# Performance work log

Hardware: AMD Instinct MI355X
Metric: run time of the kernel (lower is better)

The kernel has to match this reference:

```python
import jax, jax.numpy as jnp
import numpy as np

C0 = 256
GROUP = C0 // 32  # 8 groups, 32 channels each
K = 9             # 3x3 kernel
PAD = 1

def _layernorm(x, g, b):
    m = jnp.mean(x, -1, keepdims=True)
    v = jnp.var(x, -1, keepdims=True)
    return (x - m) * jax.lax.rsqrt(v + 1e-5) * g + b

def _dwconv(x, w, b):
    # depthwise 3x3, NHWC, kernel [3,3,1,C]
    y = jax.lax.conv_general_dilated(x, w, (1, 1), 'SAME', dimension_numbers=('NHWC', 'HWIO', 'NHWC'), feature_group_count=x.shape[-1])
    return y + b

def _bilinear(img, ix, iy):
    # img [B,Hp,Wp,c]; ix,iy [B,L] pixel coords; bilinear, zeros padding, align_corners=False
    B, Hp, Wp, c = img.shape
    flat = img.reshape(B, Hp * Wp, c)
    x0 = jnp.floor(ix)
    y0 = jnp.floor(iy)
    tx = ix - x0
    ty = iy - y0
    out = jnp.zeros(ix.shape + (c,), img.dtype)
    for dx, dy, w in ((0, 0, (1 - tx) * (1 - ty)), (1, 0, tx * (1 - ty)), (0, 1, (1 - tx) * ty), (1, 1, tx * ty)):
        xi = x0 + dx
        yi = y0 + dy
        valid = (xi >= 0) & (xi < Wp) & (yi >= 0) & (yi < Hp)
        idx = (jnp.clip(yi, 0, Hp - 1) * Wp + jnp.clip(xi, 0, Wp - 1)).astype(jnp.int32)
        v = jax.vmap(lambda f, i: f[i])(flat, idx)  # [B,L,c]
        out = out + v * (w * valid)[..., None]
    return out

def _dcnv3(x, dw_w, dw_b, ln_g, ln_b, in_w, in_b, off_w, off_b, mk_w, mk_b, out_w, out_b):
    # x: [N,H,W,C] channel-last, DCNv3 core (stride=1, dilation=1, offset_scale=1)
    N, H, W, C = x.shape
    G = GROUP
    gc = C // G
    v = x @ in_w + in_b  # input_proj (value)
    # offset/mask branch: dwconv -> LN -> GELU
    f = jax.nn.gelu(_layernorm(_dwconv(x, dw_w, dw_b), ln_g, ln_b), approximate=False)
    offset = (f @ off_w + off_b).reshape(N, H, W, G, K, 2)
    mask = jax.nn.softmax((f @ mk_w + mk_b).reshape(N, H, W, G, K), axis=-1)
    Hp = H + 2 * PAD
    Wp = W + 2 * PAD
    vp = jnp.pad(v, ((0, 0), (PAD, PAD), (PAD, PAD), (0, 0)))
    # reference points normalized by padded spatial size
    ref_x = (jnp.arange(W, dtype=x.dtype) + PAD + 0.5) / Wp
    ref_y = (jnp.arange(H, dtype=x.dtype) + PAD + 0.5) / Hp
    rx, ry = jnp.meshgrid(ref_x, ref_y, indexing='xy')  # [H,W]
    ref = jnp.stack([rx, ry], -1)  # [H,W,2] (x,y)
    k = jnp.arange(3, dtype=x.dtype) - 1.0  # [-1,0,1]
    gx, gy = jnp.meshgrid(k / Wp, k / Hp, indexing='ij')
    kgrid = jnp.stack([gx, gy], -1).reshape(K, 2)
    norm = jnp.array([Wp, Hp], dtype=x.dtype)
    loc = ref[None, :, :, None, None, :] + kgrid[None, None, None, None, :, :] + offset / norm  # [N,H,W,G,K,2]
    sg = (2.0 * loc - 1.0).transpose(0, 3, 1, 2, 4, 5).reshape(N * G, H * W * K, 2)
    ix = ((sg[..., 0] + 1.0) * Wp - 1.0) * 0.5
    iy = ((sg[..., 1] + 1.0) * Hp - 1.0) * 0.5
    imgs = vp.reshape(N, Hp, Wp, G, gc).transpose(0, 3, 1, 2, 4).reshape(N * G, Hp, Wp, gc)
    samp = _bilinear(imgs, ix, iy).reshape(N, G, H * W, K, gc)
    m = mask.transpose(0, 3, 1, 2, 4).reshape(N, G, H * W, K)
    out = jnp.einsum('nglkc,nglk->nglc', samp, m)
    out = out.transpose(0, 2, 1, 3).reshape(N, H, W, C)
    return out @ out_w + out_b

def setup_inputs() -> dict:
    key = jax.random.key(0)
    ks = iter(jax.random.split(key, 40))
    C, G = C0, GROUP
    d = {"x": jax.random.normal(next(ks), (2, C, 64, 64), jnp.float32)}
    for p in ("a", "b"):
        d[p + "_dw_w"] = jax.random.normal(next(ks), (3, 3, 1, C), jnp.float32) * 0.05
        d[p + "_dw_b"] = jnp.zeros((C,), jnp.float32)
        d[p + "_ln_g"] = jnp.ones((C,), jnp.float32)
        d[p + "_ln_b"] = jnp.zeros((C,), jnp.float32)
        d[p + "_in_w"] = jax.random.normal(next(ks), (C, C), jnp.float32) * 0.0625
        d[p + "_in_b"] = jnp.zeros((C,), jnp.float32)
        d[p + "_off_w"] = jax.random.normal(next(ks), (C, G * K * 2), jnp.float32) * 0.02
        d[p + "_off_b"] = jnp.zeros((G * K * 2,), jnp.float32)
        d[p + "_mk_w"] = jax.random.normal(next(ks), (C, G * K), jnp.float32) * 0.02
        d[p + "_mk_b"] = jnp.zeros((G * K,), jnp.float32)
        d[p + "_out_w"] = jax.random.normal(next(ks), (C, C), jnp.float32) * 0.0625
        d[p + "_out_b"] = jnp.zeros((C,), jnp.float32)
    d["proj_w"] = jax.random.normal(next(ks), (C, C), jnp.float32) * 0.0625
    d["proj_b"] = jnp.zeros((C,), jnp.float32)
    return d

def reference(x, a_dw_w, a_dw_b, a_ln_g, a_ln_b, a_in_w, a_in_b, a_off_w, a_off_b, a_mk_w, a_mk_b, a_out_w, a_out_b, b_dw_w, b_dw_b, b_ln_g, b_ln_b, b_in_w, b_in_b, b_off_w, b_off_b, b_mk_w, b_mk_b, b_out_w, b_out_b, proj_w, proj_b):
    x1 = x.transpose(0, 2, 3, 1)  # NCHW -> NHWC
    attn1 = _dcnv3(x1, a_dw_w, a_dw_b, a_ln_g, a_ln_b, a_in_w, a_in_b, a_off_w, a_off_b, a_mk_w, a_mk_b, a_out_w, a_out_b)
    attn2 = _dcnv3(attn1, b_dw_w, b_dw_b, b_ln_g, b_ln_b, b_in_w, b_in_b, b_off_w, b_off_b, b_mk_w, b_mk_b, b_out_w, b_out_b)
    attn = attn2 @ proj_w + proj_b
    return x * attn.transpose(0, 3, 1, 2)
```

## Files before the change

kernel.cpp:

```cpp
#include <hip/hip_runtime.h>
#include <hip/hip_bf16.h>
#include <math.h>

#define HH 64
#define WW 64
#define CH 256
#define NB 2
#define HWSZ (HH*WW)
#define PIX (NB*HWSZ)

typedef __attribute__((ext_vector_type(8))) short bf16x8;
typedef __attribute__((ext_vector_type(4))) float f32x4;

static __device__ __forceinline__ ushort f2bf(float f){
  union { __hip_bfloat16 h; ushort u; } cv;
  cv.h = __float2bfloat16(f);
  return cv.u;
}
static __device__ __forceinline__ float bflo(uint u){ return __uint_as_float(u << 16); }
static __device__ __forceinline__ float bfhi(uint u){ return __uint_as_float(u & 0xffff0000u); }

__global__ __launch_bounds__(256) void k_prep(const float* __restrict__ x,
    ushort* __restrict__ out16,
    const float* __restrict__ a_in_w, const float* __restrict__ a_off_w,
    const float* __restrict__ a_mk_w, const float* __restrict__ a_out_w,
    const float* __restrict__ b_in_w, const float* __restrict__ b_off_w,
    const float* __restrict__ b_mk_w, const float* __restrict__ b_out_w,
    const float* __restrict__ proj_w, ushort* __restrict__ Bt,
    const float* __restrict__ a_off_b, const float* __restrict__ a_mk_b,
    const float* __restrict__ b_off_b, const float* __restrict__ b_mk_b,
    float* __restrict__ bcatA, float* __restrict__ bcatB){
  __shared__ float t[32][33];
  int b = blockIdx.x;
  int tid = threadIdx.x;
  int tx = tid & 31, ty = tid >> 5;
  if (b < 2048) {
    int n = b >> 10, rem = b & 1023;
    int p0 = (rem & 127) * 32, c0 = (rem >> 7) * 32;
    const float* inn = x + (size_t)n * CH * HWSZ;
    ushort* o16 = out16 + (size_t)n * HWSZ * CH;
    #pragma unroll
    for (int i = 0; i < 4; ++i) {
      int c = c0 + ty + i*8;
      t[ty + i*8][tx] = inn[(size_t)c * HWSZ + p0 + tx];
    }
    __syncthreads();
    #pragma unroll
    for (int i = 0; i < 4; ++i) {
      int p = p0 + ty + i*8;
      o16[(size_t)p * CH + c0 + tx] = f2bf(t[tx][ty + i*8]);
    }
  } else if (b < 2496) {
    int zz = b - 2048;
    int z = zz >> 6, rem = zz & 63;
    int n0 = (rem & 7) * 32, k0 = (rem >> 3) * 32;
    const float* W = a_in_w; int mode = 0;
    switch(z){
      case 0: W = a_in_w; break;
      case 1: mode = 1; break;
      case 2: W = a_out_w; break;
      case 3: W = b_in_w; break;
      case 4: mode = 2; break;
      case 5: W = b_out_w; break;
      default: W = proj_w; break;
    }
    #pragma unroll
    for (int i = 0; i < 4; ++i) {
      int k = k0 + ty + i*8, nn = n0 + tx;
      float val;
      if (mode == 0) val = W[k*256 + nn];
      else {
        const float* ow = (mode == 1) ? a_off_w : b_off_w;
        const float* mw = (mode == 1) ? a_mk_w  : b_mk_w;
        val = (nn < 144) ? ow[k*144 + nn] : ((nn < 216) ? mw[k*72 + nn - 144] : 0.f);
      }
      t[ty + i*8][tx] = val;
    }
    __syncthreads();
    #pragma unroll
    for (int i = 0; i < 4; ++i) {
      int nn = n0 + ty + i*8, k = k0 + tx;
      Bt[(size_t)z*65536 + nn*256 + k] = f2bf(t[tx][ty + i*8]);
    }
  } else {
    bcatA[tid] = (tid < 144) ? a_off_b[tid] : ((tid < 216) ? a_mk_b[tid-144] : 0.f);
    bcatB[tid] = (tid < 144) ? b_off_b[tid] : ((tid < 216) ? b_mk_b[tid-144] : 0.f);
  }
}

__global__ __launch_bounds__(256) void k_dwln(const ushort* __restrict__ xin,
    const float* __restrict__ dw_w, const float* __restrict__ dw_b,
    const float* __restrict__ ln_g, const float* __restrict__ ln_b,
    ushort* __restrict__ f){
  int w_ = threadIdx.x >> 6, l = threadIdx.x & 63;
  int pix = blockIdx.x * 4 + w_;
  int c = l << 2;
  int n  = pix >> 12;
  int hw = pix & 4095;
  int h = hw >> 6, w = hw & 63;
  const ushort* xb = xin + (size_t)n * HWSZ * CH;
  float4 bv = *reinterpret_cast<const float4*>(&dw_b[c]);
  float s0 = bv.x, s1 = bv.y, s2 = bv.z, s3 = bv.w;
  #pragma unroll
  for (int i = 0; i < 3; ++i) {
    int y = h + i - 1;
    if ((unsigned)y < 64u) {
      #pragma unroll
      for (int j = 0; j < 3; ++j) {
        int x = w + j - 1;
        if ((unsigned)x < 64u) {
          uint2 xv = *reinterpret_cast<const uint2*>(&xb[((size_t)((y<<6)+x))*CH + c]);
          float4 wv = *reinterpret_cast<const float4*>(&dw_w[(i*3+j)*CH + c]);
          s0 = fmaf(bflo(xv.x), wv.x, s0);
          s1 = fmaf(bfhi(xv.x), wv.y, s1);
          s2 = fmaf(bflo(xv.y), wv.z, s2);
          s3 = fmaf(bfhi(xv.y), wv.w, s3);
        }
      }
    }
  }
  float v1 = s0 + s1 + s2 + s3;
  float v2 = s0*s0 + s1*s1 + s2*s2 + s3*s3;
  #pragma unroll
  for (int off = 32; off >= 1; off >>= 1) {
    v1 += __shfl_xor(v1, off);
    v2 += __shfl_xor(v2, off);
  }
  float mean = v1 * (1.f/256.f);
  float var  = v2 * (1.f/256.f) - mean*mean;
  float inv  = rsqrtf(var + 1e-5f);
  float4 gv = *reinterpret_cast<const float4*>(&ln_g[c]);
  float4 bb = *reinterpret_cast<const float4*>(&ln_b[c]);
  float z0 = (s0 - mean) * inv * gv.x + bb.x;
  float z1 = (s1 - mean) * inv * gv.y + bb.y;
  float z2 = (s2 - mean) * inv * gv.z + bb.z;
  float z3 = (s3 - mean) * inv * gv.w + bb.w;
  float g0 = 0.5f * z0 * (1.f + erff(z0 * 0.70710678118654752f));
  float g1 = 0.5f * z1 * (1.f + erff(z1 * 0.70710678118654752f));
  float g2 = 0.5f * z2 * (1.f + erff(z2 * 0.70710678118654752f));
  float g3 = 0.5f * z3 * (1.f + erff(z3 * 0.70710678118654752f));
  uint2 pk;
  pk.x = (uint)f2bf(g0) | ((uint)f2bf(g1) << 16);
  pk.y = (uint)f2bf(g2) | ((uint)f2bf(g3) << 16);
  *reinterpret_cast<uint2*>(&f[(size_t)pix*CH + c]) = pk;
}

template<int MODE>
static __device__ __forceinline__ void gemm_core(ushort* As, ushort* Bs,
    int rows, int by, const ushort* __restrict__ Bt, const float* __restrict__ bias,
    float* __restrict__ Cf, ushort* __restrict__ Cb,
    const float* __restrict__ xg, float* __restrict__ outg){
  int tid = threadIdx.x;
  int w = tid >> 6, l = tid & 63;
  int lr = l & 15, lk = l >> 4;
  int br = tid >> 2, bc2 = (tid & 3) << 1;
  const ushort* Bg = Bt + (size_t)(by*64 + br) * 256 + ((tid & 3) << 4);
  uint4 pb0 = *reinterpret_cast<const uint4*>(Bg);
  uint4 pb1 = *reinterpret_cast<const uint4*>(Bg + 8);
  f32x4 acc[4] = {};
  #pragma unroll
  for (int ph = 0; ph < 4; ++ph) {
    __syncthreads();
    *reinterpret_cast<uint4*>(&Bs[(br << 6) + (((bc2    ) ^ (br & 7)) << 3)]) = pb0;
    *reinterpret_cast<uint4*>(&Bs[(br << 6) + (((bc2 + 1) ^ (br & 7)) << 3)]) = pb1;
    __syncthreads();
    if (ph < 3) {
      pb0 = *reinterpret_cast<const uint4*>(Bg + (ph+1)*64);
      pb1 = *reinterpret_cast<const uint4*>(Bg + (ph+1)*64 + 8);
    }
    #pragma unroll
    for (int ks = 0; ks < 2; ++ks) {
      int col = w*16 + lr;
      bf16x8 bf = *reinterpret_cast<const bf16x8*>(&Bs[(col << 6) + ((((ks<<2) + lk) ^ (col & 7)) << 3)]);
      #pragma unroll
      for (int mi = 0; mi < 4; ++mi) {
        int row = mi*16 + lr;
        int ck = ((ph<<3) + (ks<<2) + lk) ^ (row & 31);
        bf16x8 af = *reinterpret_cast<const bf16x8*>(&As[(row << 8) + (ck << 3)]);
        acc[mi] = __builtin_amdgcn_mfma_f32_16x16x32_bf16(af, bf, acc[mi], 0, 0, 0);
      }
    }
  }
  int colg = by*64 + w*16 + lr;
  float bval = bias[colg];
  #pragma unroll
  for (int mi = 0; mi < 4; ++mi) {
    int row0 = rows + mi*16 + (lk << 2);
    if (MODE == 3) {
      int n = row0 >> 12, hw = row0 & 4095;
      size_t base = (size_t)n * (CH*HWSZ) + (size_t)colg * HWSZ + hw;
      float4 xv = *reinterpret_cast<const float4*>(&xg[base]);
      float4 ov;
      ov.x = xv.x * (acc[mi][0] + bval);
      ov.y = xv.y * (acc[mi][1] + bval);
      ov.z = xv.z * (acc[mi][2] + bval);
      ov.w = xv.w * (acc[mi][3] + bval);
      *reinterpret_cast<float4*>(&outg[base]) = ov;
    } else {
      #pragma unroll
      for (int j = 0; j < 4; ++j) {
        float val = acc[mi][j] + bval;
        if (MODE == 2) Cf[(size_t)(row0 + j) * 256 + colg] = val;
        else           Cb[(size_t)(row0 + j) * 256 + colg] = f2bf(val);
      }
    }
  }
}

static __device__ __forceinline__ void stage_A(ushort* As, const ushort* __restrict__ A, int rows){
  int tid = threadIdx.x;
  int r = tid >> 2, q0 = (tid & 3) << 3;
  const ushort* Ag = A + (size_t)(rows + r) * 256 + (q0 << 3);
  #pragma unroll
  for (int i = 0; i < 8; ++i) {
    uint4 v = *reinterpret_cast<const uint4*>(Ag + (i << 3));
    *reinterpret_cast<uint4*>(&As[(r << 8) + (((q0 + i) ^ (r & 31)) << 3)]) = v;
  }
}

template<int MODE>
__global__ __launch_bounds__(256, 4) void k_gemm256(const ushort* __restrict__ A,
    const ushort* __restrict__ Bt, const float* __restrict__ bias,
    float* __restrict__ Cf, ushort* __restrict__ Cb,
    const float* __restrict__ xg, float* __restrict__ outg){
  __shared__ ushort As[64*256];
  __shared__ ushort Bs[64*64];
  int rows = blockIdx.x * 64, by = blockIdx.y;
  stage_A(As, A, rows);
  gemm_core<MODE>(As, Bs, rows, by, Bt, bias, Cf, Cb, xg, outg);
}

__global__ __launch_bounds__(256, 4) void k_vfm(
    const ushort* __restrict__ Av, const ushort* __restrict__ Btv,
    const float* __restrict__ biasv, ushort* __restrict__ v16,
    const ushort* __restrict__ Af, const ushort* __restrict__ Btf,
    const float* __restrict__ biasf, float* __restrict__ fm32){
  __shared__ ushort As[64*256];
  __shared__ ushort Bs[64*64];
  int rows = blockIdx.x * 64, by = blockIdx.y;
  if (blockIdx.z == 0) {
    stage_A(As, Av, rows);
    gemm_core<0>(As, Bs, rows, by, Btv, biasv, nullptr, v16, nullptr, nullptr);
  } else {
    stage_A(As, Af, rows);
    gemm_core<2>(As, Bs, rows, by, Btf, biasf, fm32, nullptr, nullptr, nullptr);
  }
}

__global__ __launch_bounds__(256, 4) void k_sample(const ushort* __restrict__ v,
    const float* __restrict__ fm, ushort* __restrict__ o){
  __shared__ float sfm[4][256];
  int wv = threadIdx.x >> 6, l = threadIdx.x & 63;
  int pix = blockIdx.x * 4 + wv;
  int c = l << 2;
  int g = l >> 3;
  *reinterpret_cast<float4*>(&sfm[wv][c]) = *reinterpret_cast<const float4*>(&fm[(size_t)pix*256 + c]);
  __syncthreads();
  const float* fp = sfm[wv];
  float ml[9];
  float mx = -1e30f;
  #pragma unroll
  for (int k = 0; k < 9; ++k) { ml[k] = fp[144 + g*9 + k]; mx = fmaxf(mx, ml[k]); }
  float ssum = 0.f;
  #pragma unroll
  for (int k = 0; k < 9; ++k) { ml[k] = __expf(ml[k] - mx); ssum += ml[k]; }
  int n = pix >> 12;
  int hw = pix & 4095;
  int h = hw >> 6, w = hw & 63;
  const ushort* vb = v + (size_t)n * HWSZ * CH + c;
  float a0 = 0.f, a1 = 0.f, a2 = 0.f, a3 = 0.f;
  #pragma unroll
  for (int k = 0; k < 9; ++k) {
    int dx = k/3 - 1, dy = k%3 - 1;
    float ox = fp[g*18 + k*2];
    float oy = fp[g*18 + k*2 + 1];
    float xu = (float)(w + dx) + ox;
    float yu = (float)(h + dy) + oy;
    float xf = floorf(xu), yf = floorf(yu);
    float tx = xu - xf, ty = yu - yf;
    int x0 = (int)xf, y0 = (int)yf;
    int x1 = x0 + 1, y1 = y0 + 1;
    float m00 = (float)((unsigned)x0 < 64u && (unsigned)y0 < 64u);
    float m10 = (float)((unsigned)x1 < 64u && (unsigned)y0 < 64u);
    float m01 = (float)((unsigned)x0 < 64u && (unsigned)y1 < 64u);
    float m11 = (float)((unsigned)x1 < 64u && (unsigned)y1 < 64u);
    int xc0 = min(max(x0, 0), 63), xc1 = min(max(x1, 0), 63);
    int yc0 = min(max(y0, 0), 63), yc1 = min(max(y1, 0), 63);
    float w0x = 1.f - tx, w0y = 1.f - ty;
    uint2 q00 = *reinterpret_cast<const uint2*>(vb + (((yc0 << 6) + xc0) << 8));
    uint2 q10 = *reinterpret_cast<const uint2*>(vb + (((yc0 << 6) + xc1) << 8));
    uint2 q01 = *reinterpret_cast<const uint2*>(vb + (((yc1 << 6) + xc0) << 8));
    uint2 q11 = *reinterpret_cast<const uint2*>(vb + (((yc1 << 6) + xc1) << 8));
    float w00 = ml[k] * (w0x * w0y * m00);
    float w10 = ml[k] * (tx  * w0y * m10);
    float w01 = ml[k] * (w0x * ty  * m01);
    float w11 = ml[k] * (tx  * ty  * m11);
    a0 = fmaf(bflo(q00.x), w00, a0); a1 = fmaf(bfhi(q00.x), w00, a1);
    a2 = fmaf(bflo(q00.y), w00, a2); a3 = fmaf(bfhi(q00.y), w00, a3);
    a0 = fmaf(bflo(q10.x), w10, a0); a1 = fmaf(bfhi(q10.x), w10, a1);
    a2 = fmaf(bflo(q10.y), w10, a2); a3 = fmaf(bfhi(q10.y), w10, a3);
    a0 = fmaf(bflo(q01.x), w01, a0); a1 = fmaf(bfhi(q01.x), w01, a1);
    a2 = fmaf(bflo(q01.y), w01, a2); a3 = fmaf(bfhi(q01.y), w01, a3);
    a0 = fmaf(bflo(q11.x), w11, a0); a1 = fmaf(bfhi(q11.x), w11, a1);
    a2 = fmaf(bflo(q11.y), w11, a2); a3 = fmaf(bfhi(q11.y), w11, a3);
  }
  float inv = 1.f / ssum;
  uint2 pk;
  pk.x = (uint)f2bf(a0 * inv) | ((uint)f2bf(a1 * inv) << 16);
  pk.y = (uint)f2bf(a2 * inv) | ((uint)f2bf(a3 * inv) << 16);
  *reinterpret_cast<uint2*>(&o[(size_t)pix*256 + c]) = pk;
}

extern "C" void kernel_launch(void* const* d_in, const int* in_sizes, int n_in,
                              void* d_out, int out_size, void* d_ws, size_t ws_size,
                              hipStream_t stream) {
  const float* x      = (const float*)d_in[0];
  const float* a_dw_w = (const float*)d_in[1];
  const float* a_dw_b = (const float*)d_in[2];
  const float* a_ln_g = (const float*)d_in[3];
  const float* a_ln_b = (const float*)d_in[4];
  const float* a_in_w = (const float*)d_in[5];
  const float* a_in_b = (const float*)d_in[6];
  const float* a_off_w= (const float*)d_in[7];
  const float* a_off_b= (const float*)d_in[8];
  const float* a_mk_w = (const float*)d_in[9];
  const float* a_mk_b = (const float*)d_in[10];
  const float* a_out_w= (const float*)d_in[11];
  const float* a_out_b= (const float*)d_in[12];
  const float* b_dw_w = (const float*)d_in[13];
  const float* b_dw_b = (const float*)d_in[14];
  const float* b_ln_g = (const float*)d_in[15];
  const float* b_ln_b = (const float*)d_in[16];
  const float* b_in_w = (const float*)d_in[17];
  const float* b_in_b = (const float*)d_in[18];
  const float* b_off_w= (const float*)d_in[19];
  const float* b_off_b= (const float*)d_in[20];
  const float* b_mk_w = (const float*)d_in[21];
  const float* b_mk_b = (const float*)d_in[22];
  const float* b_out_w= (const float*)d_in[23];
  const float* b_out_b= (const float*)d_in[24];
  const float* proj_w = (const float*)d_in[25];
  const float* proj_b = (const float*)d_in[26];
  float* out = (float*)d_out;

  const size_t BUF = (size_t)PIX * CH;
  float* fm32   = (float*)d_ws;
  ushort* u = (ushort*)(fm32 + BUF);
  ushort* bx16 = u;  u += BUF;
  ushort* f16  = u;  u += BUF;
  ushort* v16  = u;  u += BUF;
  ushort* o16  = u;  u += BUF;
  ushort* a116 = u;  u += BUF;
  ushort* a216 = u;  u += BUF;
  ushort* Btw  = u;  u += (size_t)7*65536;
  float* bcatA = (float*)u;
  float* bcatB = bcatA + 256;

  dim3 gvfm(PIX/64, 4, 2);
  dim3 ggem(PIX/64, 4);

  k_prep<<<2497, 256, 0, stream>>>(x, bx16,
      a_in_w, a_off_w, a_mk_w, a_out_w, b_in_w, b_off_w, b_mk_w, b_out_w, proj_w, Btw,
      a_off_b, a_mk_b, b_off_b, b_mk_b, bcatA, bcatB);

  k_dwln<<<PIX/4, 256, 0, stream>>>(bx16, a_dw_w, a_dw_b, a_ln_g, a_ln_b, f16);
  k_vfm<<<gvfm, 256, 0, stream>>>(bx16, Btw + 0*65536, a_in_b, v16,
                                  f16, Btw + 1*65536, bcatA, fm32);
  k_sample<<<PIX/4, 256, 0, stream>>>(v16, fm32, o16);
  k_gemm256<0><<<ggem, 256, 0, stream>>>(o16, Btw + 2*65536, a_out_b, nullptr, a116, nullptr, nullptr);

  k_dwln<<<PIX/4, 256, 0, stream>>>(a116, b_dw_w, b_dw_b, b_ln_g, b_ln_b, f16);
  k_vfm<<<gvfm, 256, 0, stream>>>(a116, Btw + 3*65536, b_in_b, v16,
                                  f16, Btw + 4*65536, bcatB, fm32);
  k_sample<<<PIX/4, 256, 0, stream>>>(v16, fm32, o16);
  k_gemm256<0><<<ggem, 256, 0, stream>>>(o16, Btw + 5*65536, b_out_b, nullptr, a216, nullptr, nullptr);

  k_gemm256<3><<<ggem, 256, 0, stream>>>(a216, Btw + 6*65536, proj_b, nullptr, nullptr, x, out);
}
```

Baseline: 95.41 us.

## Fuse depthwise conv + LayerNorm + GELU into the offset/mask GEMM blocks

Removes the separate k_dwln kernel and its bf16 intermediate buffer. A fifth y-slice of the k_vfm grid now computes the dwconv/LN/GELU for its 64 pixels directly into the swizzled shared A tile, then loops over the 4 output column blocks of the offset/mask GEMM reusing that tile. This saves a global write and read of the feature map plus two launches. In exchange, one block now does four GEMM passes serially while the value-GEMM blocks do one, so load imbalance and lower parallelism for the fm branch are a risk.

```diff
diff --git a/kernel.cpp b/kernel.cpp
--- a/kernel.cpp
+++ b/kernel.cpp
@@ -88,63 +88,6 @@
   }
 }
 
-__global__ __launch_bounds__(256) void k_dwln(const ushort* __restrict__ xin,
-    const float* __restrict__ dw_w, const float* __restrict__ dw_b,
-    const float* __restrict__ ln_g, const float* __restrict__ ln_b,
-    ushort* __restrict__ f){
-  int w_ = threadIdx.x >> 6, l = threadIdx.x & 63;
-  int pix = blockIdx.x * 4 + w_;
-  int c = l << 2;
-  int n  = pix >> 12;
-  int hw = pix & 4095;
-  int h = hw >> 6, w = hw & 63;
-  const ushort* xb = xin + (size_t)n * HWSZ * CH;
-  float4 bv = *reinterpret_cast<const float4*>(&dw_b[c]);
-  float s0 = bv.x, s1 = bv.y, s2 = bv.z, s3 = bv.w;
-  #pragma unroll
-  for (int i = 0; i < 3; ++i) {
-    int y = h + i - 1;
-    if ((unsigned)y < 64u) {
-      #pragma unroll
-      for (int j = 0; j < 3; ++j) {
-        int x = w + j - 1;
-        if ((unsigned)x < 64u) {
-          uint2 xv = *reinterpret_cast<const uint2*>(&xb[((size_t)((y<<6)+x))*CH + c]);
-          float4 wv = *reinterpret_cast<const float4*>(&dw_w[(i*3+j)*CH + c]);
-          s0 = fmaf(bflo(xv.x), wv.x, s0);
-          s1 = fmaf(bfhi(xv.x), wv.y, s1);
-          s2 = fmaf(bflo(xv.y), wv.z, s2);
-          s3 = fmaf(bfhi(xv.y), wv.w, s3);
-        }
-      }
-    }
-  }
-  float v1 = s0 + s1 + s2 + s3;
-  float v2 = s0*s0 + s1*s1 + s2*s2 + s3*s3;
-  #pragma unroll
-  for (int off = 32; off >= 1; off >>= 1) {
-    v1 += __shfl_xor(v1, off);
-    v2 += __shfl_xor(v2, off);
-  }
-  float mean = v1 * (1.f/256.f);
-  float var  = v2 * (1.f/256.f) - mean*mean;
-  float inv  = rsqrtf(var + 1e-5f);
-  float4 gv = *reinterpret_cast<const float4*>(&ln_g[c]);
-  float4 bb = *reinterpret_cast<const float4*>(&ln_b[c]);
-  float z0 = (s0 - mean) * inv * gv.x + bb.x;
-  float z1 = (s1 - mean) * inv * gv.y + bb.y;
-  float z2 = (s2 - mean) * inv * gv.z + bb.z;
-  float z3 = (s3 - mean) * inv * gv.w + bb.w;
-  float g0 = 0.5f * z0 * (1.f + erff(z0 * 0.70710678118654752f));
-  float g1 = 0.5f * z1 * (1.f + erff(z1 * 0.70710678118654752f));
-  float g2 = 0.5f * z2 * (1.f + erff(z2 * 0.70710678118654752f));
-  float g3 = 0.5f * z3 * (1.f + erff(z3 * 0.70710678118654752f));
-  uint2 pk;
-  pk.x = (uint)f2bf(g0) | ((uint)f2bf(g1) << 16);
-  pk.y = (uint)f2bf(g2) | ((uint)f2bf(g3) << 16);
-  *reinterpret_cast<uint2*>(&f[(size_t)pix*CH + c]) = pk;
-}
-
 template<int MODE>
 static __device__ __forceinline__ void gemm_core(ushort* As, ushort* Bs,
     int rows, int by, const ushort* __restrict__ Bt, const float* __restrict__ bias,
@@ -231,19 +174,76 @@
 }
 
 __global__ __launch_bounds__(256, 4) void k_vfm(
-    const ushort* __restrict__ Av, const ushort* __restrict__ Btv,
-    const float* __restrict__ biasv, ushort* __restrict__ v16,
-    const ushort* __restrict__ Af, const ushort* __restrict__ Btf,
-    const float* __restrict__ biasf, float* __restrict__ fm32){
+    const ushort* __restrict__ xin,
+    const float* __restrict__ dw_w, const float* __restrict__ dw_b,
+    const float* __restrict__ ln_g, const float* __restrict__ ln_b,
+    const ushort* __restrict__ Btv, const float* __restrict__ biasv, ushort* __restrict__ v16,
+    const ushort* __restrict__ Btf, const float* __restrict__ biasf, float* __restrict__ fm32){
   __shared__ ushort As[64*256];
   __shared__ ushort Bs[64*64];
   int rows = blockIdx.x * 64, by = blockIdx.y;
-  if (blockIdx.z == 0) {
-    stage_A(As, Av, rows);
+  if (by < 4) {
+    stage_A(As, xin, rows);
     gemm_core<0>(As, Bs, rows, by, Btv, biasv, nullptr, v16, nullptr, nullptr);
   } else {
-    stage_A(As, Af, rows);
-    gemm_core<2>(As, Bs, rows, by, Btf, biasf, fm32, nullptr, nullptr, nullptr);
+    int wv = threadIdx.x >> 6, l = threadIdx.x & 63;
+    int c = l << 2;
+    for (int it = 0; it < 16; ++it) {
+      int lrow = it*4 + wv;
+      int pix = rows + lrow;
+      int n  = pix >> 12;
+      int hw = pix & 4095;
+      int h = hw >> 6, w = hw & 63;
+      const ushort* xb = xin + (size_t)n * HWSZ * CH;
+      float4 bv = *reinterpret_cast<const float4*>(&dw_b[c]);
+      float s0 = bv.x, s1 = bv.y, s2 = bv.z, s3 = bv.w;
+      #pragma unroll
+      for (int i = 0; i < 3; ++i) {
+        int y = h + i - 1;
+        if ((unsigned)y < 64u) {
+          #pragma unroll
+          for (int j = 0; j < 3; ++j) {
+            int xx = w + j - 1;
+            if ((unsigned)xx < 64u) {
+              uint2 xv = *reinterpret_cast<const uint2*>(&xb[((size_t)((y<<6)+xx))*CH + c]);
+              float4 wv4 = *reinterpret_cast<const float4*>(&dw_w[(i*3+j)*CH + c]);
+              s0 = fmaf(bflo(xv.x), wv4.x, s0);
+              s1 = fmaf(bfhi(xv.x), wv4.y, s1);
+              s2 = fmaf(bflo(xv.y), wv4.z, s2);
+              s3 = fmaf(bfhi(xv.y), wv4.w, s3);
+            }
+          }
+        }
+      }
+      float v1 = s0 + s1 + s2 + s3;
+      float v2 = s0*s0 + s1*s1 + s2*s2 + s3*s3;
+      #pragma unroll
+      for (int off = 32; off >= 1; off >>= 1) {
+        v1 += __shfl_xor(v1, off);
+        v2 += __shfl_xor(v2, off);
+      }
+      float mean = v1 * (1.f/256.f);
+      float var  = v2 * (1.f/256.f) - mean*mean;
+      float inv  = rsqrtf(var + 1e-5f);
+      float4 gv = *reinterpret_cast<const float4*>(&ln_g[c]);
+      float4 bb = *reinterpret_cast<const float4*>(&ln_b[c]);
+      float z0 = (s0 - mean) * inv * gv.x + bb.x;
+      float z1 = (s1 - mean) * inv * gv.y + bb.y;
+      float z2 = (s2 - mean) * inv * gv.z + bb.z;
+      float z3 = (s3 - mean) * inv * gv.w + bb.w;
+      float g0 = 0.5f * z0 * (1.f + erff(z0 * 0.70710678118654752f));
+      float g1 = 0.5f * z1 * (1.f + erff(z1 * 0.70710678118654752f));
+      float g2 = 0.5f * z2 * (1.f + erff(z2 * 0.70710678118654752f));
+      float g3 = 0.5f * z3 * (1.f + erff(z3 * 0.70710678118654752f));
+      uint2 pk;
+      pk.x = (uint)f2bf(g0) | ((uint)f2bf(g1) << 16);
+      pk.y = (uint)f2bf(g2) | ((uint)f2bf(g3) << 16);
+      *reinterpret_cast<uint2*>(&As[(lrow << 8) + ((((l >> 1) ^ (lrow & 31))) << 3) + ((l & 1) << 2)]) = pk;
+    }
+    __syncthreads();
+    #pragma unroll 1
+    for (int cb = 0; cb < 4; ++cb)
+      gemm_core<2>(As, Bs, rows, cb, Btf, biasf, fm32, nullptr, nullptr, nullptr);
   }
 }
 
@@ -347,7 +347,6 @@
   float* fm32   = (float*)d_ws;
   ushort* u = (ushort*)(fm32 + BUF);
   ushort* bx16 = u;  u += BUF;
-  ushort* f16  = u;  u += BUF;
   ushort* v16  = u;  u += BUF;
   ushort* o16  = u;  u += BUF;
   ushort* a116 = u;  u += BUF;
@@ -356,22 +355,22 @@
   float* bcatA = (float*)u;
   float* bcatB = bcatA + 256;
 
-  dim3 gvfm(PIX/64, 4, 2);
+  dim3 gvfm(PIX/64, 5);
   dim3 ggem(PIX/64, 4);
 
   k_prep<<<2497, 256, 0, stream>>>(x, bx16,
       a_in_w, a_off_w, a_mk_w, a_out_w, b_in_w, b_off_w, b_mk_w, b_out_w, proj_w, Btw,
       a_off_b, a_mk_b, b_off_b, b_mk_b, bcatA, bcatB);
 
-  k_dwln<<<PIX/4, 256, 0, stream>>>(bx16, a_dw_w, a_dw_b, a_ln_g, a_ln_b, f16);
-  k_vfm<<<gvfm, 256, 0, stream>>>(bx16, Btw + 0*65536, a_in_b, v16,
-                                  f16, Btw + 1*65536, bcatA, fm32);
+  k_vfm<<<gvfm, 256, 0, stream>>>(bx16, a_dw_w, a_dw_b, a_ln_g, a_ln_b,
+                                  Btw + 0*65536, a_in_b, v16,
+                                  Btw + 1*65536, bcatA, fm32);
   k_sample<<<PIX/4, 256, 0, stream>>>(v16, fm32, o16);
   k_gemm256<0><<<ggem, 256, 0, stream>>>(o16, Btw + 2*65536, a_out_b, nullptr, a116, nullptr, nullptr);
 
-  k_dwln<<<PIX/4, 256, 0, stream>>>(a116, b_dw_w, b_dw_b, b_ln_g, b_ln_b, f16);
-  k_vfm<<<gvfm, 256, 0, stream>>>(a116, Btw + 3*65536, b_in_b, v16,
-                                  f16, Btw + 4*65536, bcatB, fm32);
+  k_vfm<<<gvfm, 256, 0, stream>>>(a116, b_dw_w, b_dw_b, b_ln_g, b_ln_b,
+                                  Btw + 3*65536, b_in_b, v16,
+                                  Btw + 4*65536, bcatB, fm32);
   k_sample<<<PIX/4, 256, 0, stream>>>(v16, fm32, o16);
   k_gemm256<0><<<ggem, 256, 0, stream>>>(o16, Btw + 5*65536, b_out_b, nullptr, a216, nullptr, nullptr);
 
```

Measured after the change: 162.0 us. 1.7x slower.
